# Kernel optimization log

Measured on AMD Instinct MI355X. Metric: run time of the kernel, lower is better.

Reference implementation:

```python
import jax, jax.numpy as jnp
import numpy as np

C = 32          # in/out channels per spnn.Conv3d(32, 32, 2, stride=2)
KVOL = 8        # 2^3 kernel offsets
GRID = 128      # voxel grid resolution
N_RAW = 1_000_000


def setup_inputs() -> dict:
    rng = np.random.default_rng(0)
    # unique active voxel coordinates (torchsparse coords are unique)
    coords = np.unique(rng.integers(0, GRID, size=(N_RAW, 3), dtype=np.int32), axis=0)
    n = coords.shape[0]
    # kernel=2, stride=2: each input voxel hits exactly one output voxel
    out_coords = coords // 2
    k_idx = (coords[:, 0] % 2) * 4 + (coords[:, 1] % 2) * 2 + (coords[:, 2] % 2)
    _, out_idx = np.unique(out_coords, axis=0, return_inverse=True)
    num_out = int(out_idx.max()) + 1

    key = jax.random.key(0)
    kx, kw = jax.random.split(key)
    x = jax.random.normal(kx, (n, C), dtype=jnp.float32)
    W = jax.random.normal(kw, (KVOL, C, C), dtype=jnp.float32) * 0.05
    return {
        "x": x,
        "W": W,
        "k_idx": jnp.asarray(k_idx, dtype=jnp.int32),
        "out_idx": jnp.asarray(out_idx, dtype=jnp.int32),
        "num_out": num_out,
    }


def reference(x, W, k_idx, out_idx, num_out):
    # gather -> per-offset GEMM -> scatter-add (sparse conv kernel-map form)
    # proj[n, k, d] = sum_c x[n, c] * W[k, c, d]
    proj = jnp.einsum("nc,kcd->nkd", x, W)
    # pick the projection for each point's kernel offset: [n, C]
    sel = jnp.take_along_axis(proj, k_idx[:, None, None], axis=1)[:, 0, :]
    # scatter-add into output voxels
    out = jax.ops.segment_sum(sel, out_idx, num_segments=num_out)
    return out
```

## Files before the change

### kernel.cpp

```cpp
#include <hip/hip_runtime.h>
#include <hip/hip_bf16.h>


typedef __attribute__((ext_vector_type(8))) short bf16x8;
typedef __attribute__((ext_vector_type(4))) float f32x4;

union ABFrag { bf16x8 v; int i[4]; };
union BFI { __hip_bfloat162 h; int i; };

__device__ __forceinline__ int pack2_bf16(float a, float b) {
    BFI u; u.h = __float22bfloat162_rn(make_float2(a, b));
    return u.i;
}

__device__ __forceinline__ unsigned short f2bf(float f) {
    union { float f; unsigned u; } v; v.f = f;
    unsigned r = v.u + 0x7FFFu + ((v.u >> 16) & 1u);
    return (unsigned short)(r >> 16);
}

__global__ __launch_bounds__(256) void prep_fill_kernel(
    const float* __restrict__ W, unsigned short* __restrict__ WB,
    int4* __restrict__ child4, int n4) {
    int t = blockIdx.x * blockDim.x + threadIdx.x;
    if (t < 8 * 2 * 64 * 8) {
        int j    = t & 7;
        int lane = (t >> 3) & 63;
        int half = (t >> 9) & 1;
        int k    = t >> 10;
        int c = (lane >> 4) * 8 + j;
        int d = half * 16 + (lane & 15);
        WB[t] = f2bf(W[k * 1024 + c * 32 + d]);
    }
    const int4 m1 = make_int4(-1, -1, -1, -1);
    for (int i = t; i < n4; i += gridDim.x * blockDim.x) child4[i] = m1;
}

__global__ __launch_bounds__(256) void build_map_kernel(
    const int* __restrict__ k_idx, const int* __restrict__ out_idx,
    int* __restrict__ child, int n) {
    int t = blockIdx.x * blockDim.x + threadIdx.x;
    if (t < n) child[(size_t)out_idx[t] * 8 + k_idx[t]] = t;
}

__global__ __launch_bounds__(256, 4) void conv_gather_kernel(
    const float* __restrict__ x,
    const unsigned short* __restrict__ WB,
    const int* __restrict__ child,
    float* __restrict__ out,
    int num_out)
{
    const int lane  = threadIdx.x & 63;
    const int wv    = threadIdx.x >> 6;
    const int obase = (blockIdx.x * 4 + wv) * 16;
    if (obase >= num_out) return;

    const int row  = lane & 15;
    const int quad = lane >> 4;
    int o = obase + row;
    if (o >= num_out) o = num_out - 1;

    const int4* cp = (const int4*)(child + (size_t)o * 8);
    int4 c0 = cp[0], c1 = cp[1];
    int pk[8] = {c0.x, c0.y, c0.z, c0.w, c1.x, c1.y, c1.z, c1.w};

    const float* xp0[8];
#pragma unroll
    for (int k = 0; k < 8; ++k) {
        int p = pk[k] < 0 ? 0 : pk[k];
        xp0[k] = x + (size_t)p * 32 + quad * 8;
    }
    float4 xa[8], xb[8];
#pragma unroll
    for (int k = 0; k < 8; ++k) {
        xa[k] = *(const float4*)(xp0[k]);
        xb[k] = *(const float4*)(xp0[k] + 4);
    }

    f32x4 acc0 = {0.f, 0.f, 0.f, 0.f};
    f32x4 acc1 = {0.f, 0.f, 0.f, 0.f};

#pragma unroll
    for (int k = 0; k < 8; ++k) {
        const bool valid = pk[k] >= 0;
        ABFrag a;
        a.i[0] = valid ? pack2_bf16(xa[k].x, xa[k].y) : 0;
        a.i[1] = valid ? pack2_bf16(xa[k].z, xa[k].w) : 0;
        a.i[2] = valid ? pack2_bf16(xb[k].x, xb[k].y) : 0;
        a.i[3] = valid ? pack2_bf16(xb[k].z, xb[k].w) : 0;
        bf16x8 b0 = *(const bf16x8*)(WB + ((size_t)(k * 2 + 0) * 64 + lane) * 8);
        bf16x8 b1 = *(const bf16x8*)(WB + ((size_t)(k * 2 + 1) * 64 + lane) * 8);
        acc0 = __builtin_amdgcn_mfma_f32_16x16x32_bf16(a.v, b0, acc0, 0, 0, 0);
        acc1 = __builtin_amdgcn_mfma_f32_16x16x32_bf16(a.v, b1, acc1, 0, 0, 0);
    }

#pragma unroll
    for (int r = 0; r < 4; ++r) {
        int oo = obase + quad * 4 + r;
        if (oo < num_out) {
            float* op = out + (size_t)oo * 32 + (lane & 15);
            op[0]  = acc0[r];
            op[16] = acc1[r];
        }
    }
}

__global__ void prep_w_kernel(const float* __restrict__ W,
                              unsigned short* __restrict__ WB) {
    int t = blockIdx.x * blockDim.x + threadIdx.x;
    if (t >= 8 * 2 * 64 * 8) return;
    int j = t & 7, lane = (t >> 3) & 63, half = (t >> 9) & 1, k = t >> 10;
    int c = (lane >> 4) * 8 + j;
    int d = half * 16 + (lane & 15);
    WB[t] = f2bf(W[k * 1024 + c * 32 + d]);
}

__global__ __launch_bounds__(256) void conv_atomic_kernel(
    const float* __restrict__ x, const unsigned short* __restrict__ WB,
    const int* __restrict__ k_idx, const int* __restrict__ out_idx,
    float* __restrict__ out, int n)
{
    const int lane = threadIdx.x & 63;
    const int wv   = threadIdx.x >> 6;
    const int base = (blockIdx.x * 4 + wv) * 16;
    if (base >= n) return;
    const int row = lane & 15, quad = lane >> 4;
    const int p = base + row;
    int krow = -1;
    ABFrag a; a.i[0] = a.i[1] = a.i[2] = a.i[3] = 0;
    if (p < n) {
        krow = k_idx[p];
        const float* xp = x + (size_t)p * 32 + quad * 8;
        float4 x0 = *(const float4*)xp;
        float4 x1 = *(const float4*)(xp + 4);
        a.i[0] = pack2_bf16(x0.x, x0.y);
        a.i[1] = pack2_bf16(x0.z, x0.w);
        a.i[2] = pack2_bf16(x1.x, x1.y);
        a.i[3] = pack2_bf16(x1.z, x1.w);
    }
    f32x4 acc0 = {0.f,0.f,0.f,0.f}, acc1 = {0.f,0.f,0.f,0.f};
#pragma unroll
    for (int k = 0; k < 8; ++k) {
        bf16x8 b0 = *(const bf16x8*)(WB + ((size_t)(k*2+0)*64 + lane)*8);
        bf16x8 b1 = *(const bf16x8*)(WB + ((size_t)(k*2+1)*64 + lane)*8);
        const bool keep = (krow == k);
        ABFrag ak;
        ak.i[0] = keep ? a.i[0] : 0; ak.i[1] = keep ? a.i[1] : 0;
        ak.i[2] = keep ? a.i[2] : 0; ak.i[3] = keep ? a.i[3] : 0;
        acc0 = __builtin_amdgcn_mfma_f32_16x16x32_bf16(ak.v, b0, acc0, 0, 0, 0);
        acc1 = __builtin_amdgcn_mfma_f32_16x16x32_bf16(ak.v, b1, acc1, 0, 0, 0);
    }
#pragma unroll
    for (int r = 0; r < 4; ++r) {
        int p2 = base + quad * 4 + r;
        if (p2 < n) {
            int oi = out_idx[p2];
            float* op = out + (size_t)oi * 32 + (lane & 15);
            atomicAdd(op,      acc0[r]);
            atomicAdd(op + 16, acc1[r]);
        }
    }
}

extern "C" void kernel_launch(void* const* d_in, const int* in_sizes, int n_in,
                              void* d_out, int out_size, void* d_ws, size_t ws_size,
                              hipStream_t stream) {
    const float* x       = (const float*)d_in[0];
    const float* W       = (const float*)d_in[1];
    const int*   k_idx   = (const int*)d_in[2];
    const int*   out_idx = (const int*)d_in[3];
    const int n = in_sizes[2];
    const int num_out = out_size / 32;
    float* out = (float*)d_out;

    unsigned short* WB = (unsigned short*)d_ws;
    const size_t wb_bytes = 16384;
    int* child = (int*)((char*)d_ws + wb_bytes);
    const size_t child_bytes = (size_t)num_out * 8 * sizeof(int);

    if (ws_size >= wb_bytes + child_bytes) {
        int n4 = num_out * 2;
        int blocksA = (n4 + 255) / 256;
        if (blocksA < 32) blocksA = 32;
        prep_fill_kernel<<<blocksA, 256, 0, stream>>>(W, WB, (int4*)child, n4);
        build_map_kernel<<<(n + 255) / 256, 256, 0, stream>>>(k_idx, out_idx, child, n);
        int blocks = (num_out + 63) / 64;
        conv_gather_kernel<<<blocks, 256, 0, stream>>>(x, WB, child, out, num_out);
    } else {
        prep_w_kernel<<<32, 256, 0, stream>>>(W, WB);
        hipMemsetAsync(d_out, 0, (size_t)out_size * sizeof(float), stream);
        int blocks = (n + 63) / 64;
        conv_atomic_kernel<<<blocks, 256, 0, stream>>>(x, WB, k_idx, out_idx, out, n);
    }
}
```

Baseline: 183.9 us.

## Convert gather conv to persistent grid-stride strips with XCD-aware block swizzle

Replaces the one-wave-per-16-outputs launch with a fixed 1024-block persistent grid. Each wave loops over strips of four 16-output tiles and prefetches all child indices for the strip up front. Block IDs are swizzled across groups of eight, apparently to spread neighbouring work across XCDs. The goal is to cut launch and tail overhead and overlap index loads with the gathers. In exchange, launch bounds drop to 2 blocks per SM, which raises register pressure and may reduce latency hiding for the random x gathers.

Result: no change. 185.8 us (+1.0%).

```diff
diff --git a/kernel.cpp b/kernel.cpp
--- a/kernel.cpp
+++ b/kernel.cpp
@@ -43,64 +43,75 @@
     if (t < n) child[(size_t)out_idx[t] * 8 + k_idx[t]] = t;
 }
 
-__global__ __launch_bounds__(256, 4) void conv_gather_kernel(
+#define T_STRIP 4
+
+__global__ __launch_bounds__(256, 2) void conv_gather_kernel(
     const float* __restrict__ x,
     const unsigned short* __restrict__ WB,
     const int* __restrict__ child,
     float* __restrict__ out,
-    int num_out)
+    int num_out, int nStrips)
 {
-    const int lane  = threadIdx.x & 63;
-    const int wv    = threadIdx.x >> 6;
-    const int obase = (blockIdx.x * 4 + wv) * 16;
-    if (obase >= num_out) return;
-
+    const int lane = threadIdx.x & 63;
+    const int wv   = threadIdx.x >> 6;
     const int row  = lane & 15;
     const int quad = lane >> 4;
-    int o = obase + row;
-    if (o >= num_out) o = num_out - 1;
-
-    const int4* cp = (const int4*)(child + (size_t)o * 8);
-    int4 c0 = cp[0], c1 = cp[1];
-    int pk[8] = {c0.x, c0.y, c0.z, c0.w, c1.x, c1.y, c1.z, c1.w};
-
-    const float* xp0[8];
-#pragma unroll
-    for (int k = 0; k < 8; ++k) {
-        int p = pk[k] < 0 ? 0 : pk[k];
-        xp0[k] = x + (size_t)p * 32 + quad * 8;
-    }
-    float4 xa[8], xb[8];
-#pragma unroll
-    for (int k = 0; k < 8; ++k) {
-        xa[k] = *(const float4*)(xp0[k]);
-        xb[k] = *(const float4*)(xp0[k] + 4);
-    }
-
-    f32x4 acc0 = {0.f, 0.f, 0.f, 0.f};
-    f32x4 acc1 = {0.f, 0.f, 0.f, 0.f};
-
-#pragma unroll
-    for (int k = 0; k < 8; ++k) {
-        const bool valid = pk[k] >= 0;
-        ABFrag a;
-        a.i[0] = valid ? pack2_bf16(xa[k].x, xa[k].y) : 0;
-        a.i[1] = valid ? pack2_bf16(xa[k].z, xa[k].w) : 0;
-        a.i[2] = valid ? pack2_bf16(xb[k].x, xb[k].y) : 0;
-        a.i[3] = valid ? pack2_bf16(xb[k].z, xb[k].w) : 0;
-        bf16x8 b0 = *(const bf16x8*)(WB + ((size_t)(k * 2 + 0) * 64 + lane) * 8);
-        bf16x8 b1 = *(const bf16x8*)(WB + ((size_t)(k * 2 + 1) * 64 + lane) * 8);
-        acc0 = __builtin_amdgcn_mfma_f32_16x16x32_bf16(a.v, b0, acc0, 0, 0, 0);
-        acc1 = __builtin_amdgcn_mfma_f32_16x16x32_bf16(a.v, b1, acc1, 0, 0, 0);
-    }
-
-#pragma unroll
-    for (int r = 0; r < 4; ++r) {
-        int oo = obase + quad * 4 + r;
-        if (oo < num_out) {
-            float* op = out + (size_t)oo * 32 + (lane & 15);
-            op[0]  = acc0[r];
-            op[16] = acc1[r];
+
+    const int nb  = gridDim.x;
+    const int bid = (int)blockIdx.x;
+    const int sw  = (bid & 7) * (nb >> 3) + (bid >> 3);
+    const int waveStride = nb * 4;
+
+    for (int sid = sw * 4 + wv; sid < nStrips; sid += waveStride) {
+        int pk[T_STRIP][8];
+#pragma unroll
+        for (int j = 0; j < T_STRIP; ++j) {
+            int o = (sid * T_STRIP + j) * 16 + row;
+            if (o >= num_out) o = num_out - 1;
+            const int4* cp = (const int4*)(child + (size_t)o * 8);
+            int4 c0 = cp[0], c1 = cp[1];
+            pk[j][0] = c0.x; pk[j][1] = c0.y; pk[j][2] = c0.z; pk[j][3] = c0.w;
+            pk[j][4] = c1.x; pk[j][5] = c1.y; pk[j][6] = c1.z; pk[j][7] = c1.w;
+        }
+
+#pragma unroll
+        for (int j = 0; j < T_STRIP; ++j) {
+            const int obase = (sid * T_STRIP + j) * 16;
+
+            float4 xa[8], xb[8];
+#pragma unroll
+            for (int k = 0; k < 8; ++k) {
+                int p = pk[j][k] < 0 ? 0 : pk[j][k];
+                const float* xp = x + (size_t)p * 32 + quad * 8;
+                xa[k] = *(const float4*)xp;
+                xb[k] = *(const float4*)(xp + 4);
+            }
+
+            f32x4 acc0 = {0.f, 0.f, 0.f, 0.f};
+            f32x4 acc1 = {0.f, 0.f, 0.f, 0.f};
+#pragma unroll
+            for (int k = 0; k < 8; ++k) {
+                const bool valid = pk[j][k] >= 0;
+                ABFrag a;
+                a.i[0] = valid ? pack2_bf16(xa[k].x, xa[k].y) : 0;
+                a.i[1] = valid ? pack2_bf16(xa[k].z, xa[k].w) : 0;
+                a.i[2] = valid ? pack2_bf16(xb[k].x, xb[k].y) : 0;
+                a.i[3] = valid ? pack2_bf16(xb[k].z, xb[k].w) : 0;
+                bf16x8 b0 = *(const bf16x8*)(WB + ((size_t)(k * 2 + 0) * 64 + lane) * 8);
+                bf16x8 b1 = *(const bf16x8*)(WB + ((size_t)(k * 2 + 1) * 64 + lane) * 8);
+                acc0 = __builtin_amdgcn_mfma_f32_16x16x32_bf16(a.v, b0, acc0, 0, 0, 0);
+                acc1 = __builtin_amdgcn_mfma_f32_16x16x32_bf16(a.v, b1, acc1, 0, 0, 0);
+            }
+
+#pragma unroll
+            for (int r = 0; r < 4; ++r) {
+                int oo = obase + quad * 4 + r;
+                if (oo < num_out) {
+                    float* op = out + (size_t)oo * 32 + row;
+                    op[0]  = acc0[r];
+                    op[16] = acc1[r];
+                }
+            }
         }
     }
 }
@@ -184,8 +195,11 @@
         if (blocksA < 32) blocksA = 32;
         prep_fill_kernel<<<blocksA, 256, 0, stream>>>(W, WB, (int4*)child, n4);
         build_map_kernel<<<(n + 255) / 256, 256, 0, stream>>>(k_idx, out_idx, child, n);
-        int blocks = (num_out + 63) / 64;
-        conv_gather_kernel<<<blocks, 256, 0, stream>>>(x, WB, child, out, num_out);
+
+        int nTiles  = (num_out + 15) / 16;
+        int nStrips = (nTiles + T_STRIP - 1) / T_STRIP;
+        conv_gather_kernel<<<1024, 256, 0, stream>>>(x, WB, child, out,
+                                                     num_out, nStrips);
     } else {
         prep_w_kernel<<<32, 256, 0, stream>>>(W, WB);
         hipMemsetAsync(d_out, 0, (size_t)out_size * sizeof(float), stream);
```
